# Performance work log

Measured on AMD Instinct MI355X. Metric: run time of the kernel, lower is better.

The kernel has to match this reference:

```python
import jax, jax.numpy as jnp
import numpy as np

B, T, D, HD = 4, 4096, 1024, 64

def setup_inputs() -> dict:
    key = jax.random.key(0)
    k1, k2, k3, k4 = jax.random.split(key, 4)
    scale = 1.0 / np.sqrt(D)
    return {
        "x": jax.random.normal(k1, (B, T, D), dtype=jnp.float32),
        "Wq": jax.random.normal(k2, (HD, D), dtype=jnp.float32) * scale,
        "Wk": jax.random.normal(k3, (HD, D), dtype=jnp.float32) * scale,
        "Wv": jax.random.normal(k4, (HD, D), dtype=jnp.float32) * scale,
    }

def reference(x, Wq, Wk, Wv):
    # x: [B,T,D]; W*: [head_dim, D] (torch Linear weight layout)
    Q = jnp.einsum('btd,hd->bth', x, Wq)  # [B,T,HD]
    K = jnp.einsum('btd,hd->bth', x, Wk)
    V = jnp.einsum('btd,hd->bth', x, Wv)
    hd = Q.shape[-1]
    scores = jnp.einsum('bqh,bkh->bqk', Q, K) * (hd ** -0.5)  # [B,T,T]
    t = scores.shape[1]
    causal = jnp.tril(jnp.ones((t, t), dtype=bool))
    scores = jnp.where(causal, scores, -jnp.inf)
    att = jax.nn.softmax(scores, axis=-1)
    return jnp.einsum('bqk,bkh->bqh', att, V)  # [B,T,HD]
```

## Files before the change

### kernel.cpp

```cpp
#include <hip/hip_runtime.h>
#include <stdint.h>

#define B_  4
#define T_  4096
#define D_  1024
#define HD_ 64
#define BT_ 16384

typedef short bf16x8 __attribute__((ext_vector_type(8)));
typedef float f32x4  __attribute__((ext_vector_type(4)));
typedef unsigned short u16;
typedef u16 u16x4 __attribute__((ext_vector_type(4)));
typedef unsigned int u32;
typedef u32 u32x4 __attribute__((ext_vector_type(4)));

#define M0_   8.0f
#define L2E_  1.44269504f
#define M0L2_ 11.54156032f

#define SLOTS_B_ 288

__device__ __forceinline__ u16 f2bf(float f) {
    union { float f; unsigned u; } v; v.f = f;
    unsigned r = (v.u + 0x7FFF + ((v.u >> 16) & 1)) >> 16;
    return (u16)r;
}
__device__ __forceinline__ float bf2f(u16 u) {
    union { unsigned u; float f; } v; v.u = ((unsigned)u) << 16;
    return v.f;
}
__device__ __forceinline__ u32 cvt_pk_bf16(float lo, float hi) {
    u32 r;
    asm("v_cvt_pk_bf16_f32 %0, %1, %2" : "=v"(r) : "v"(lo), "v"(hi));
    return r;
}

__device__ __forceinline__ int slot_base(int qt) {
    int a = qt >> 3, r = qt & 7;
    return qt + 4 * a * (a - 1) + a * r;
}

__global__ __launch_bounds__(256) void wconv_kernel(
    const float* __restrict__ wq, const float* __restrict__ wk,
    const float* __restrict__ wv, u16* __restrict__ wb)
{
    const int j   = blockIdx.x >> 5;
    const int off = (blockIdx.x & 31) * 2048 + threadIdx.x * 8;
    const float* src = (j == 0) ? wq : ((j == 1) ? wk : wv);
    f32x4 a0 = *(const f32x4*)(src + off);
    f32x4 a1 = *(const f32x4*)(src + off + 4);
    u32x4 b;
    b[0] = cvt_pk_bf16(a0[0], a0[1]);
    b[1] = cvt_pk_bf16(a0[2], a0[3]);
    b[2] = cvt_pk_bf16(a1[0], a1[1]);
    b[3] = cvt_pk_bf16(a1[2], a1[3]);
    *(u32x4*)(wb + j * 65536 + off) = b;
}

__global__ __launch_bounds__(256) void qkv_kernel(
    const float* __restrict__ x, const u16* __restrict__ wb,
    u16* __restrict__ qs, u16* __restrict__ kss, u16* __restrict__ vssT)
{
    __shared__ __align__(16) u16 xt[32][72];
    __shared__ __align__(16) u16 wt[192][72];

    const int tid  = threadIdx.x;
    const int lane = tid & 63;
    const int w    = tid >> 6;
    const int quad = lane >> 4;
    const int l16  = lane & 15;
    const int row0 = blockIdx.x * 32;
    const int sp   = w >> 1;
    const int gh   = (w & 1) * 6;

    const int xrow = tid >> 3;
    const int xcg  = tid & 7;

    f32x4 acc[6];
    #pragma unroll
    for (int g = 0; g < 6; ++g) acc[g] = (f32x4)0.0f;

    f32x4 xa, xb;
    bf16x8 wr[6];
    {
        const float* xp = x + (size_t)(row0 + xrow) * D_ + xcg * 8;
        xa = *(const f32x4*)xp; xb = *(const f32x4*)(xp + 4);
        #pragma unroll
        for (int i = 0; i < 6; ++i) {
            int chunk = tid + 256 * i;
            wr[i] = *(const bf16x8*)(wb + (size_t)(chunk >> 3) * D_ + (chunk & 7) * 8);
        }
    }

    for (int kc = 0; kc < 16; ++kc) {
        __syncthreads();
        {
            u32x4 px;
            px[0] = cvt_pk_bf16(xa[0], xa[1]);
            px[1] = cvt_pk_bf16(xa[2], xa[3]);
            px[2] = cvt_pk_bf16(xb[0], xb[1]);
            px[3] = cvt_pk_bf16(xb[2], xb[3]);
            *(u32x4*)&xt[xrow][xcg * 8] = px;
            #pragma unroll
            for (int i = 0; i < 6; ++i) {
                int chunk = tid + 256 * i;
                *(bf16x8*)&wt[chunk >> 3][(chunk & 7) * 8] = wr[i];
            }
        }
        __syncthreads();
        if (kc < 15) {
            const float* xp = x + (size_t)(row0 + xrow) * D_ + (kc + 1) * 64 + xcg * 8;
            xa = *(const f32x4*)xp; xb = *(const f32x4*)(xp + 4);
            #pragma unroll
            for (int i = 0; i < 6; ++i) {
                int chunk = tid + 256 * i;
                wr[i] = *(const bf16x8*)(wb + (size_t)(chunk >> 3) * D_ + (kc + 1) * 64 + (chunk & 7) * 8);
            }
        }
        #pragma unroll
        for (int ks = 0; ks < 2; ++ks) {
            bf16x8 a = *(const bf16x8*)&xt[sp * 16 + l16][ks * 32 + quad * 8];
            #pragma unroll
            for (int g = 0; g < 6; ++g) {
                bf16x8 b = *(const bf16x8*)&wt[(gh + g) * 16 + l16][ks * 32 + quad * 8];
                acc[g] = __builtin_amdgcn_mfma_f32_16x16x32_bf16(a, b, acc[g], 0, 0, 0);
            }
        }
    }
    #pragma unroll
    for (int g = 0; g < 6; ++g) {
        const int n = (gh + g) * 16 + l16;
        const int j = n >> 6, h = n & 63;
        const int rbase = row0 + sp * 16 + quad * 4;
        if (j == 0) {
            #pragma unroll
            for (int r = 0; r < 4; ++r) qs[(size_t)(rbase + r) * HD_ + h] = f2bf(acc[g][r] * 0.125f);
        } else if (j == 1) {
            #pragma unroll
            for (int r = 0; r < 4; ++r) kss[(size_t)(rbase + r) * HD_ + h] = f2bf(acc[g][r]);
        } else {
            u16x4 v;
            #pragma unroll
            for (int r = 0; r < 4; ++r) v[r] = f2bf(acc[g][r]);
            *(u16x4*)(vssT + (size_t)h * BT_ + rbase) = v;
        }
    }
}

__global__ __launch_bounds__(256) void attn_kernel(
    const u16* __restrict__ qs, const u16* __restrict__ kss,
    const u16* __restrict__ vssT,
    float* __restrict__ pl, u16* __restrict__ pO)
{
    __shared__ __align__(16) u16 kt[64][72];
    __shared__ __align__(16) u16 vt[80][72];
    __shared__ __align__(16) u16 pt[4][16][72];

    const int bi = blockIdx.x;
    const int c  = bi & 7;
    const int qt = (bi >> 3) & 63;
    const int b  = bi >> 9;
    if ((c << 3) > qt) return;

    const int kt0  = c << 3;
    const int kend = ((kt0 + 7) < qt) ? (kt0 + 7) : qt;

    const int tid  = threadIdx.x;
    const int lane = tid & 63;
    const int w    = tid >> 6;
    const int quad = lane >> 4;
    const int l16  = lane & 15;
    const int qb   = qt * 64;
    const size_t base = (size_t)b * T_;

    for (int idx = tid; idx < 16 * 72; idx += 256) {
        int rr = idx / 72, cc = idx - rr * 72;
        vt[64 + rr][cc] = (rr == 0) ? (u16)0x3F80 : (u16)0;
    }

    bf16x8 qf[2];
    {
        const u16* qp = qs + (base + qb + w * 16 + l16) * HD_ + quad * 8;
        qf[0] = *(const bf16x8*)(qp);
        qf[1] = *(const bf16x8*)(qp + 32);
    }

    f32x4 o_acc[5];
    #pragma unroll
    for (int g = 0; g < 5; ++g) o_acc[g] = (f32x4)0.0f;

    const int lr = tid >> 2, lp = tid & 3;

    bf16x8 kr0, kr1, vr0, vr1;
    {
        const u16* sk = kss + (base + kt0 * 64 + lr) * HD_ + lp * 16;
        kr0 = *(const bf16x8*)(sk);  kr1 = *(const bf16x8*)(sk + 8);
        const u16* sv = vssT + (size_t)lr * BT_ + base + kt0 * 64 + lp * 16;
        vr0 = *(const bf16x8*)(sv);  vr1 = *(const bf16x8*)(sv + 8);
    }

    for (int kti = kt0; kti <= kend; ++kti) {
        __syncthreads();
        *(bf16x8*)&kt[lr][lp * 16]     = kr0;
        *(bf16x8*)&kt[lr][lp * 16 + 8] = kr1;
        *(bf16x8*)&vt[lr][lp * 16]     = vr0;
        *(bf16x8*)&vt[lr][lp * 16 + 8] = vr1;
        __syncthreads();
        if (kti < kend) {
            const u16* sk = kss + (base + (kti + 1) * 64 + lr) * HD_ + lp * 16;
            kr0 = *(const bf16x8*)(sk);  kr1 = *(const bf16x8*)(sk + 8);
            const u16* sv = vssT + (size_t)lr * BT_ + base + (kti + 1) * 64 + lp * 16;
            vr0 = *(const bf16x8*)(sv);  vr1 = *(const bf16x8*)(sv + 8);
        }

        f32x4 s[4];
        #pragma unroll
        for (int g = 0; g < 4; ++g) {
            s[g] = (f32x4)0.0f;
            #pragma unroll
            for (int ks = 0; ks < 2; ++ks) {
                bf16x8 kf = *(const bf16x8*)&kt[g * 16 + l16][ks * 32 + quad * 8];
                s[g] = __builtin_amdgcn_mfma_f32_16x16x32_bf16(qf[ks], kf, s[g], 0, 0, 0);
            }
        }
        if (kti == qt) {
            #pragma unroll
            for (int g = 0; g < 4; ++g) {
                int key = kti * 64 + g * 16 + l16;
                #pragma unroll
                for (int r = 0; r < 4; ++r) {
                    int q = qb + w * 16 + quad * 4 + r;
                    if (key > q) s[g][r] = -1e30f;
                }
            }
        }
        #pragma unroll
        for (int g = 0; g < 4; ++g) {
            #pragma unroll
            for (int r = 0; r < 4; r += 2) {
                float e0 = __builtin_amdgcn_exp2f(s[g][r]     * L2E_ - M0L2_);
                float e1 = __builtin_amdgcn_exp2f(s[g][r + 1] * L2E_ - M0L2_);
                u32 pk = cvt_pk_bf16(e0, e1);
                pt[w][quad * 4 + r][g * 16 + l16]     = (u16)pk;
                pt[w][quad * 4 + r + 1][g * 16 + l16] = (u16)(pk >> 16);
            }
        }
        #pragma unroll
        for (int ks = 0; ks < 2; ++ks) {
            bf16x8 pa = *(const bf16x8*)&pt[w][l16][ks * 32 + quad * 8];
            #pragma unroll
            for (int g = 0; g < 5; ++g) {
                bf16x8 vf = *(const bf16x8*)&vt[g * 16 + l16][ks * 32 + quad * 8];
                o_acc[g] = __builtin_amdgcn_mfma_f32_16x16x32_bf16(pa, vf, o_acc[g], 0, 0, 0);
            }
        }
    }

    const int slot = b * SLOTS_B_ + slot_base(qt) + c;
    if (l16 == 0) {
        #pragma unroll
        for (int r = 0; r < 4; ++r)
            pl[slot * 64 + w * 16 + quad * 4 + r] = o_acc[4][r];
    }
    #pragma unroll
    for (int g = 0; g < 4; ++g) {
        #pragma unroll
        for (int r = 0; r < 4; ++r) {
            int row = w * 16 + quad * 4 + r;
            pO[(size_t)slot * 4096 + row * 64 + g * 16 + l16] = f2bf(o_acc[g][r]);
        }
    }
}

__global__ __launch_bounds__(256) void merge_kernel(
    const float* __restrict__ pl, const u16* __restrict__ pO,
    float* __restrict__ out)
{
    const int bi = blockIdx.x;
    const int rh = bi & 1;
    const int qt = (bi >> 1) & 63;
    const int b  = bi >> 7;
    const int nc = (qt >> 3) + 1;
    const int s0 = b * SLOTS_B_ + slot_base(qt);
    const int row = rh * 32 + (threadIdx.x >> 3);
    const int hg  = (threadIdx.x & 7) * 8;

    float L = 0.0f;
    for (int c2 = 0; c2 < nc; ++c2) L += pl[(s0 + c2) * 64 + row];

    float o[8];
    #pragma unroll
    for (int i = 0; i < 8; ++i) o[i] = 0.0f;
    for (int c2 = 0; c2 < nc; ++c2) {
        const u16* p = pO + (size_t)(s0 + c2) * 4096 + row * 64 + hg;
        bf16x8 v0 = *(const bf16x8*)p;
        #pragma unroll
        for (int i = 0; i < 8; ++i) o[i] += bf2f((u16)v0[i]);
    }
    const float inv = 1.0f / L;
    float* op = out + ((size_t)b * T_ + qt * 64 + row) * HD_ + hg;
    f32x4 v;
    #pragma unroll
    for (int i = 0; i < 4; ++i) v[i] = o[i] * inv;
    *(f32x4*)op = v;
    #pragma unroll
    for (int i = 0; i < 4; ++i) v[i] = o[4 + i] * inv;
    *(f32x4*)(op + 4) = v;
}

extern "C" void kernel_launch(void* const* d_in, const int* in_sizes, int n_in,
                              void* d_out, int out_size, void* d_ws, size_t ws_size,
                              hipStream_t stream) {
    const float* x  = (const float*)d_in[0];
    const float* wq = (const float*)d_in[1];
    const float* wk = (const float*)d_in[2];
    const float* wv = (const float*)d_in[3];

    const size_t NE = (size_t)BT_ * HD_;
    char* ws = (char*)d_ws;
    u16* qs   = (u16*)ws;
    u16* kss  = qs  + NE;
    u16* vssT = kss + NE;
    u16* wb   = vssT + NE;
    float* pl = (float*)(wb + 192 * 1024);
    u16* pO   = (u16*)(pl + 4 * SLOTS_B_ * 64);
    float* out = (float*)d_out;

    wconv_kernel<<<dim3(96),   dim3(256), 0, stream>>>(wq, wk, wv, wb);
    qkv_kernel  <<<dim3(512),  dim3(256), 0, stream>>>(x, wb, qs, kss, vssT);
    attn_kernel <<<dim3(2048), dim3(256), 0, stream>>>(qs, kss, vssT, pl, pO);
    merge_kernel<<<dim3(512),  dim3(256), 0, stream>>>(pl, pO, out);
}
```

Baseline: 154.1 us.

## Load K/V MFMA fragments directly into registers, drop shared-memory staging

Each wave now loads its K and V MFMA operands straight from global memory into registers instead of staging them through shared K/V tiles. This removes two block-wide barriers per key tile. K for the next tile is prefetched after the QK MFMAs, and the all-ones row-sum column becomes a register constant. The log2(e) factor is folded into the Q scaling so the exponent needs one fewer multiply, and setprio hints are placed around the MFMA groups. In exchange, each of the four waves reloads the same K/V data from global/L2 (about 4x redundant traffic) and register pressure rises, and V loads are issued only at the start of each iteration.

```diff
diff --git a/kernel.cpp b/kernel.cpp
--- a/kernel.cpp
+++ b/kernel.cpp
@@ -14,9 +14,10 @@
 typedef unsigned int u32;
 typedef u32 u32x4 __attribute__((ext_vector_type(4)));
 
-#define M0_   8.0f
-#define L2E_  1.44269504f
-#define M0L2_ 11.54156032f
+#define M0_    8.0f
+#define L2E_   1.44269504f
+#define M0L2_  11.54156032f
+#define QSCALE_ 0.18033688f
 
 #define SLOTS_B_ 288
 
@@ -134,7 +135,7 @@
         const int rbase = row0 + sp * 16 + quad * 4;
         if (j == 0) {
             #pragma unroll
-            for (int r = 0; r < 4; ++r) qs[(size_t)(rbase + r) * HD_ + h] = f2bf(acc[g][r] * 0.125f);
+            for (int r = 0; r < 4; ++r) qs[(size_t)(rbase + r) * HD_ + h] = f2bf(acc[g][r] * QSCALE_);
         } else if (j == 1) {
             #pragma unroll
             for (int r = 0; r < 4; ++r) kss[(size_t)(rbase + r) * HD_ + h] = f2bf(acc[g][r]);
@@ -152,8 +153,6 @@
     const u16* __restrict__ vssT,
     float* __restrict__ pl, u16* __restrict__ pO)
 {
-    __shared__ __align__(16) u16 kt[64][72];
-    __shared__ __align__(16) u16 vt[80][72];
     __shared__ __align__(16) u16 pt[4][16][72];
 
     const int bi = blockIdx.x;
@@ -173,11 +172,6 @@
     const int qb   = qt * 64;
     const size_t base = (size_t)b * T_;
 
-    for (int idx = tid; idx < 16 * 72; idx += 256) {
-        int rr = idx / 72, cc = idx - rr * 72;
-        vt[64 + rr][cc] = (rr == 0) ? (u16)0x3F80 : (u16)0;
-    }
-
     bf16x8 qf[2];
     {
         const u16* qp = qs + (base + qb + w * 16 + l16) * HD_ + quad * 8;
@@ -185,44 +179,52 @@
         qf[1] = *(const bf16x8*)(qp + 32);
     }
 
+    bf16x8 vf4;
+    {
+        const short o = (l16 == 0) ? (short)0x3F80 : (short)0;
+        #pragma unroll
+        for (int i = 0; i < 8; ++i) vf4[i] = o;
+    }
+
     f32x4 o_acc[5];
     #pragma unroll
     for (int g = 0; g < 5; ++g) o_acc[g] = (f32x4)0.0f;
 
-    const int lr = tid >> 2, lp = tid & 3;
-
-    bf16x8 kr0, kr1, vr0, vr1;
-    {
-        const u16* sk = kss + (base + kt0 * 64 + lr) * HD_ + lp * 16;
-        kr0 = *(const bf16x8*)(sk);  kr1 = *(const bf16x8*)(sk + 8);
-        const u16* sv = vssT + (size_t)lr * BT_ + base + kt0 * 64 + lp * 16;
-        vr0 = *(const bf16x8*)(sv);  vr1 = *(const bf16x8*)(sv + 8);
-    }
+    const u16* kfp = kss  + (base + l16) * HD_ + quad * 8;
+    const u16* vfp = vssT + (size_t)l16 * BT_ + base + quad * 8;
+
+    bf16x8 kfr[8], vfr[8];
+    #pragma unroll
+    for (int g = 0; g < 4; ++g)
+        #pragma unroll
+        for (int ks = 0; ks < 2; ++ks)
+            kfr[g * 2 + ks] = *(const bf16x8*)(kfp + (size_t)(kt0 * 64 + g * 16) * HD_ + ks * 32);
 
     for (int kti = kt0; kti <= kend; ++kti) {
-        __syncthreads();
-        *(bf16x8*)&kt[lr][lp * 16]     = kr0;
-        *(bf16x8*)&kt[lr][lp * 16 + 8] = kr1;
-        *(bf16x8*)&vt[lr][lp * 16]     = vr0;
-        *(bf16x8*)&vt[lr][lp * 16 + 8] = vr1;
-        __syncthreads();
-        if (kti < kend) {
-            const u16* sk = kss + (base + (kti + 1) * 64 + lr) * HD_ + lp * 16;
-            kr0 = *(const bf16x8*)(sk);  kr1 = *(const bf16x8*)(sk + 8);
-            const u16* sv = vssT + (size_t)lr * BT_ + base + (kti + 1) * 64 + lp * 16;
-            vr0 = *(const bf16x8*)(sv);  vr1 = *(const bf16x8*)(sv + 8);
-        }
+        #pragma unroll
+        for (int g = 0; g < 4; ++g)
+            #pragma unroll
+            for (int ks = 0; ks < 2; ++ks)
+                vfr[g * 2 + ks] = *(const bf16x8*)(vfp + (size_t)g * 16 * BT_ + kti * 64 + ks * 32);
 
         f32x4 s[4];
+        __builtin_amdgcn_s_setprio(1);
         #pragma unroll
         for (int g = 0; g < 4; ++g) {
             s[g] = (f32x4)0.0f;
-            #pragma unroll
-            for (int ks = 0; ks < 2; ++ks) {
-                bf16x8 kf = *(const bf16x8*)&kt[g * 16 + l16][ks * 32 + quad * 8];
-                s[g] = __builtin_amdgcn_mfma_f32_16x16x32_bf16(qf[ks], kf, s[g], 0, 0, 0);
-            }
-        }
+            s[g] = __builtin_amdgcn_mfma_f32_16x16x32_bf16(qf[0], kfr[g * 2 + 0], s[g], 0, 0, 0);
+            s[g] = __builtin_amdgcn_mfma_f32_16x16x32_bf16(qf[1], kfr[g * 2 + 1], s[g], 0, 0, 0);
+        }
+        __builtin_amdgcn_s_setprio(0);
+
+        if (kti < kend) {
+            #pragma unroll
+            for (int g = 0; g < 4; ++g)
+                #pragma unroll
+                for (int ks = 0; ks < 2; ++ks)
+                    kfr[g * 2 + ks] = *(const bf16x8*)(kfp + (size_t)((kti + 1) * 64 + g * 16) * HD_ + ks * 32);
+        }
+
         if (kti == qt) {
             #pragma unroll
             for (int g = 0; g < 4; ++g) {
@@ -238,8 +240,8 @@
         for (int g = 0; g < 4; ++g) {
             #pragma unroll
             for (int r = 0; r < 4; r += 2) {
-                float e0 = __builtin_amdgcn_exp2f(s[g][r]     * L2E_ - M0L2_);
-                float e1 = __builtin_amdgcn_exp2f(s[g][r + 1] * L2E_ - M0L2_);
+                float e0 = __builtin_amdgcn_exp2f(s[g][r]     - M0L2_);
+                float e1 = __builtin_amdgcn_exp2f(s[g][r + 1] - M0L2_);
                 u32 pk = cvt_pk_bf16(e0, e1);
                 pt[w][quad * 4 + r][g * 16 + l16]     = (u16)pk;
                 pt[w][quad * 4 + r + 1][g * 16 + l16] = (u16)(pk >> 16);
@@ -248,11 +250,12 @@
         #pragma unroll
         for (int ks = 0; ks < 2; ++ks) {
             bf16x8 pa = *(const bf16x8*)&pt[w][l16][ks * 32 + quad * 8];
-            #pragma unroll
-            for (int g = 0; g < 5; ++g) {
-                bf16x8 vf = *(const bf16x8*)&vt[g * 16 + l16][ks * 32 + quad * 8];
-                o_acc[g] = __builtin_amdgcn_mfma_f32_16x16x32_bf16(pa, vf, o_acc[g], 0, 0, 0);
-            }
+            __builtin_amdgcn_s_setprio(1);
+            #pragma unroll
+            for (int g = 0; g < 4; ++g)
+                o_acc[g] = __builtin_amdgcn_mfma_f32_16x16x32_bf16(pa, vfr[g * 2 + ks], o_acc[g], 0, 0, 0);
+            o_acc[4] = __builtin_amdgcn_mfma_f32_16x16x32_bf16(pa, vf4, o_acc[4], 0, 0, 0);
+            __builtin_amdgcn_s_setprio(0);
         }
     }
 
```

Measured after the change: 235.9 us. 1.53x slower.

## Share K/V tiles across two query tiles per 512-thread attention block

Applied to the files above, without the earlier changes.

The attention kernel now processes two adjacent 64-row query tiles per block with 8 waves, so each staged K/V tile in shared memory serves twice as many queries and global loads are halved. K and V staging is split across thread halves. The log2(e) factor is folded into the Q pre-scale so the exp2 argument needs one fewer multiply, and s_setprio is placed around the MFMA sections. Costs include idle waves on the diagonal tile for the lower query tile, a larger block with more barrier participants, and roughly double the LDS for the P buffer.

```diff
diff --git a/kernel.cpp b/kernel.cpp
--- a/kernel.cpp
+++ b/kernel.cpp
@@ -14,9 +14,8 @@
 typedef unsigned int u32;
 typedef u32 u32x4 __attribute__((ext_vector_type(4)));
 
-#define M0_   8.0f
-#define L2E_  1.44269504f
-#define M0L2_ 11.54156032f
+#define M0L2_  11.54156032f
+#define QSCALE_ 0.18033688f
 
 #define SLOTS_B_ 288
 
@@ -134,7 +133,7 @@
         const int rbase = row0 + sp * 16 + quad * 4;
         if (j == 0) {
             #pragma unroll
-            for (int r = 0; r < 4; ++r) qs[(size_t)(rbase + r) * HD_ + h] = f2bf(acc[g][r] * 0.125f);
+            for (int r = 0; r < 4; ++r) qs[(size_t)(rbase + r) * HD_ + h] = f2bf(acc[g][r] * QSCALE_);
         } else if (j == 1) {
             #pragma unroll
             for (int r = 0; r < 4; ++r) kss[(size_t)(rbase + r) * HD_ + h] = f2bf(acc[g][r]);
@@ -147,40 +146,42 @@
     }
 }
 
-__global__ __launch_bounds__(256) void attn_kernel(
+__global__ __launch_bounds__(512, 6) void attn_kernel(
     const u16* __restrict__ qs, const u16* __restrict__ kss,
     const u16* __restrict__ vssT,
     float* __restrict__ pl, u16* __restrict__ pO)
 {
     __shared__ __align__(16) u16 kt[64][72];
     __shared__ __align__(16) u16 vt[80][72];
-    __shared__ __align__(16) u16 pt[4][16][72];
-
-    const int bi = blockIdx.x;
-    const int c  = bi & 7;
-    const int qt = (bi >> 3) & 63;
-    const int b  = bi >> 9;
-    if ((c << 3) > qt) return;
+    __shared__ __align__(16) u16 pt[8][16][72];
+
+    const int bi  = blockIdx.x;
+    const int c   = bi & 7;
+    const int qt2 = (bi >> 3) & 31;
+    const int b   = bi >> 8;
+    const int qthi = qt2 * 2 + 1;
+    if ((c << 3) > qthi) return;
 
     const int kt0  = c << 3;
-    const int kend = ((kt0 + 7) < qt) ? (kt0 + 7) : qt;
+    const int kend = ((kt0 + 7) < qthi) ? (kt0 + 7) : qthi;
 
     const int tid  = threadIdx.x;
     const int lane = tid & 63;
     const int w    = tid >> 6;
     const int quad = lane >> 4;
     const int l16  = lane & 15;
-    const int qb   = qt * 64;
+    const int qtw  = qt2 * 2 + (w >> 2);
+    const int wr   = (w & 3) * 16;
     const size_t base = (size_t)b * T_;
 
-    for (int idx = tid; idx < 16 * 72; idx += 256) {
+    for (int idx = tid; idx < 16 * 72; idx += 512) {
         int rr = idx / 72, cc = idx - rr * 72;
         vt[64 + rr][cc] = (rr == 0) ? (u16)0x3F80 : (u16)0;
     }
 
     bf16x8 qf[2];
     {
-        const u16* qp = qs + (base + qb + w * 16 + l16) * HD_ + quad * 8;
+        const u16* qp = qs + (base + qtw * 64 + wr + l16) * HD_ + quad * 8;
         qf[0] = *(const bf16x8*)(qp);
         qf[1] = *(const bf16x8*)(qp + 32);
     }
@@ -189,84 +190,91 @@
     #pragma unroll
     for (int g = 0; g < 5; ++g) o_acc[g] = (f32x4)0.0f;
 
-    const int lr = tid >> 2, lp = tid & 3;
-
-    bf16x8 kr0, kr1, vr0, vr1;
-    {
-        const u16* sk = kss + (base + kt0 * 64 + lr) * HD_ + lp * 16;
-        kr0 = *(const bf16x8*)(sk);  kr1 = *(const bf16x8*)(sk + 8);
-        const u16* sv = vssT + (size_t)lr * BT_ + base + kt0 * 64 + lp * 16;
-        vr0 = *(const bf16x8*)(sv);  vr1 = *(const bf16x8*)(sv + 8);
-    }
+    const int  lr  = (tid & 255) >> 2;
+    const int  lp  = tid & 3;
+    const bool isV = tid >= 256;
+
+    const u16* sp = isV ? (vssT + (size_t)lr * BT_ + base + kt0 * 64 + lp * 16)
+                        : (kss + (base + kt0 * 64 + lr) * HD_ + lp * 16);
+    const ptrdiff_t step = isV ? 64 : 64 * HD_;
+    u16* dst = isV ? &vt[lr][lp * 16] : &kt[lr][lp * 16];
+
+    bf16x8 r0 = *(const bf16x8*)(sp);
+    bf16x8 r1 = *(const bf16x8*)(sp + 8);
+    sp += step;
 
     for (int kti = kt0; kti <= kend; ++kti) {
         __syncthreads();
-        *(bf16x8*)&kt[lr][lp * 16]     = kr0;
-        *(bf16x8*)&kt[lr][lp * 16 + 8] = kr1;
-        *(bf16x8*)&vt[lr][lp * 16]     = vr0;
-        *(bf16x8*)&vt[lr][lp * 16 + 8] = vr1;
+        *(bf16x8*)(dst)     = r0;
+        *(bf16x8*)(dst + 8) = r1;
         __syncthreads();
         if (kti < kend) {
-            const u16* sk = kss + (base + (kti + 1) * 64 + lr) * HD_ + lp * 16;
-            kr0 = *(const bf16x8*)(sk);  kr1 = *(const bf16x8*)(sk + 8);
-            const u16* sv = vssT + (size_t)lr * BT_ + base + (kti + 1) * 64 + lp * 16;
-            vr0 = *(const bf16x8*)(sv);  vr1 = *(const bf16x8*)(sv + 8);
-        }
-
-        f32x4 s[4];
-        #pragma unroll
-        for (int g = 0; g < 4; ++g) {
-            s[g] = (f32x4)0.0f;
+            r0 = *(const bf16x8*)(sp);
+            r1 = *(const bf16x8*)(sp + 8);
+            sp += step;
+        }
+
+        if (kti <= qtw) {
+            f32x4 s[4];
+            __builtin_amdgcn_s_setprio(1);
+            #pragma unroll
+            for (int g = 0; g < 4; ++g) {
+                s[g] = (f32x4)0.0f;
+                #pragma unroll
+                for (int ks = 0; ks < 2; ++ks) {
+                    bf16x8 kf = *(const bf16x8*)&kt[g * 16 + l16][ks * 32 + quad * 8];
+                    s[g] = __builtin_amdgcn_mfma_f32_16x16x32_bf16(qf[ks], kf, s[g], 0, 0, 0);
+                }
+            }
+            __builtin_amdgcn_s_setprio(0);
+
+            if (kti == qtw) {
+                #pragma unroll
+                for (int g = 0; g < 4; ++g) {
+                    int key = kti * 64 + g * 16 + l16;
+                    #pragma unroll
+                    for (int r = 0; r < 4; ++r) {
+                        int q = qtw * 64 + wr + quad * 4 + r;
+                        if (key > q) s[g][r] = -1e30f;
+                    }
+                }
+            }
+            #pragma unroll
+            for (int g = 0; g < 4; ++g) {
+                #pragma unroll
+                for (int r = 0; r < 4; r += 2) {
+                    float e0 = __builtin_amdgcn_exp2f(s[g][r]     - M0L2_);
+                    float e1 = __builtin_amdgcn_exp2f(s[g][r + 1] - M0L2_);
+                    u32 pk = cvt_pk_bf16(e0, e1);
+                    pt[w][quad * 4 + r][g * 16 + l16]     = (u16)pk;
+                    pt[w][quad * 4 + r + 1][g * 16 + l16] = (u16)(pk >> 16);
+                }
+            }
             #pragma unroll
             for (int ks = 0; ks < 2; ++ks) {
-                bf16x8 kf = *(const bf16x8*)&kt[g * 16 + l16][ks * 32 + quad * 8];
-                s[g] = __builtin_amdgcn_mfma_f32_16x16x32_bf16(qf[ks], kf, s[g], 0, 0, 0);
-            }
-        }
-        if (kti == qt) {
-            #pragma unroll
-            for (int g = 0; g < 4; ++g) {
-                int key = kti * 64 + g * 16 + l16;
+                bf16x8 pa = *(const bf16x8*)&pt[w][l16][ks * 32 + quad * 8];
+                __builtin_amdgcn_s_setprio(1);
                 #pragma unroll
-                for (int r = 0; r < 4; ++r) {
-                    int q = qb + w * 16 + quad * 4 + r;
-                    if (key > q) s[g][r] = -1e30f;
+                for (int g = 0; g < 5; ++g) {
+                    bf16x8 vf = *(const bf16x8*)&vt[g * 16 + l16][ks * 32 + quad * 8];
+                    o_acc[g] = __builtin_amdgcn_mfma_f32_16x16x32_bf16(pa, vf, o_acc[g], 0, 0, 0);
                 }
-            }
-        }
-        #pragma unroll
-        for (int g = 0; g < 4; ++g) {
-            #pragma unroll
-            for (int r = 0; r < 4; r += 2) {
-                float e0 = __builtin_amdgcn_exp2f(s[g][r]     * L2E_ - M0L2_);
-                float e1 = __builtin_amdgcn_exp2f(s[g][r + 1] * L2E_ - M0L2_);
-                u32 pk = cvt_pk_bf16(e0, e1);
-                pt[w][quad * 4 + r][g * 16 + l16]     = (u16)pk;
-                pt[w][quad * 4 + r + 1][g * 16 + l16] = (u16)(pk >> 16);
-            }
-        }
-        #pragma unroll
-        for (int ks = 0; ks < 2; ++ks) {
-            bf16x8 pa = *(const bf16x8*)&pt[w][l16][ks * 32 + quad * 8];
-            #pragma unroll
-            for (int g = 0; g < 5; ++g) {
-                bf16x8 vf = *(const bf16x8*)&vt[g * 16 + l16][ks * 32 + quad * 8];
-                o_acc[g] = __builtin_amdgcn_mfma_f32_16x16x32_bf16(pa, vf, o_acc[g], 0, 0, 0);
-            }
-        }
-    }
-
-    const int slot = b * SLOTS_B_ + slot_base(qt) + c;
+                __builtin_amdgcn_s_setprio(0);
+            }
+        }
+    }
+
+    const int slot = b * SLOTS_B_ + slot_base(qtw) + c;
     if (l16 == 0) {
         #pragma unroll
         for (int r = 0; r < 4; ++r)
-            pl[slot * 64 + w * 16 + quad * 4 + r] = o_acc[4][r];
+            pl[slot * 64 + wr + quad * 4 + r] = o_acc[4][r];
     }
     #pragma unroll
     for (int g = 0; g < 4; ++g) {
         #pragma unroll
         for (int r = 0; r < 4; ++r) {
-            int row = w * 16 + quad * 4 + r;
+            int row = wr + quad * 4 + r;
             pO[(size_t)slot * 4096 + row * 64 + g * 16 + l16] = f2bf(o_acc[g][r]);
         }
     }
@@ -328,6 +336,6 @@
 
     wconv_kernel<<<dim3(96),   dim3(256), 0, stream>>>(wq, wk, wv, wb);
     qkv_kernel  <<<dim3(512),  dim3(256), 0, stream>>>(x, wb, qs, kss, vssT);
-    attn_kernel <<<dim3(2048), dim3(256), 0, stream>>>(qs, kss, vssT, pl, pO);
+    attn_kernel <<<dim3(1024), dim3(512), 0, stream>>>(qs, kss, vssT, pl, pO);
     merge_kernel<<<dim3(512),  dim3(256), 0, stream>>>(pl, pO, out);
 }
```

Result: no change. 155.9 us (+1.2%).
